# Optimization experiments

Measured on AMD Instinct MI355X. Metric: run time of the kernel, lower is better.

Reference implementation:

```python
import jax, jax.numpy as jnp
import numpy as np

N_CLASS = 12
N_OVO = N_CLASS * (N_CLASS - 1) // 2  # 66
_I_IDX, _J_IDX = np.triu_indices(N_CLASS, k=1)  # static pair -> (winner_if_pos, winner_if_neg)


def _resize_bilinear(x, size):
    # torch F.interpolate(mode='bilinear', align_corners=False) == jax half-pixel bilinear
    return jax.image.resize(x, (x.shape[0], x.shape[1], size, size), method='bilinear')


def _vote(o):
    # o: [N, n_ovo, H, W] pairwise logits -> [N, n_class, H, W] vote counts
    v = (o > 0).astype(o.dtype)                 # 1 where class i beats class j
    vt = jnp.swapaxes(v, 0, 1)                  # [P, N, H, W], pair axis leading
    res = (jax.ops.segment_sum(vt, jnp.asarray(_I_IDX), num_segments=N_CLASS)
           + jax.ops.segment_sum(1.0 - vt, jnp.asarray(_J_IDX), num_segments=N_CLASS))
    return jnp.swapaxes(res, 0, 1)              # [N, n_class, H, W]


def setup_inputs() -> dict:
    key = jax.random.key(0)
    ks = jax.random.split(key, 12)
    dims = [512, 256, 128, 64]
    sizes = [32, 64, 128, 256]
    N = 8
    inp = {}
    for i, (d, s) in enumerate(zip(dims, sizes)):
        inp[f"stage{i}"] = jax.random.normal(ks[i], (N, d, s, s), dtype=jnp.float32)
        inp[f"w{i}"] = jax.random.normal(ks[4 + i], (N_OVO, d), dtype=jnp.float32) * 0.05
        inp[f"b{i}"] = jax.random.normal(ks[8 + i], (N_OVO,), dtype=jnp.float32) * 0.05
    inp["last_only"] = 1
    return inp


def reference(stage0, stage1, stage2, stage3, w0, w1, w2, w3, b0, b1, b2, b3, last_only):
    stages = [stage0, stage1, stage2, stage3]
    ws = [w0, w1, w2, w3]
    bs = [b0, b1, b2, b3]
    # 1x1 convs: [N,C,H,W] x [O,C] -> [N,O,H,W]
    outputs = [jnp.einsum('nchw,oc->nohw', s, w) + b[None, :, None, None]
               for s, w, b in zip(stages, ws, bs)]
    if last_only:
        size = stages[-1].shape[2]
        total = outputs[0] * 0  # placeholder shape via sum below
        layers = [_resize_bilinear(o, size) for o in outputs]
        acc = layers[0]
        for l in layers[1:]:
            acc = acc + l
        outputs = [acc]
    else:
        for i in range(1, len(stages)):
            size = stages[i].shape[2]
            acc = outputs[i]
            for o in outputs[:i]:
                acc = acc + _resize_bilinear(o, size)
            outputs.append(acc)
    voted = tuple(_vote(o) for o in outputs)
    return voted[0] if last_only else voted
```

## Files before the change

### kernel.cpp

```cpp
#include <hip/hip_runtime.h>
#include <cstdint>
#include <cstddef>


#define N_BATCH 8
#define N_OVO   66
#define N_CLS   12

__constant__ unsigned char PAIR_I[N_OVO] = {
  0,0,0,0,0,0,0,0,0,0,0,
  1,1,1,1,1,1,1,1,1,1,
  2,2,2,2,2,2,2,2,2,
  3,3,3,3,3,3,3,3,
  4,4,4,4,4,4,4,
  5,5,5,5,5,5,
  6,6,6,6,6,
  7,7,7,7,
  8,8,8,
  9,9,
  10
};
__constant__ unsigned char PAIR_J[N_OVO] = {
  1,2,3,4,5,6,7,8,9,10,11,
  2,3,4,5,6,7,8,9,10,11,
  3,4,5,6,7,8,9,10,11,
  4,5,6,7,8,9,10,11,
  5,6,7,8,9,10,11,
  6,7,8,9,10,11,
  7,8,9,10,11,
  8,9,10,11,
  9,10,11,
  10,11,
  11
};

template<int C, int S2, int OG>
__device__ __forceinline__
void conv_body(int b, const float* __restrict__ x, const float* __restrict__ w,
               const float* __restrict__ bias, float* __restrict__ out)
{
    constexpr int NOG = N_OVO / OG;
    constexpr int PX  = S2 / 256;
    const int og  = b % NOG;
    int rest      = b / NOG;
    const int pxb = rest % PX;
    const int n   = rest / PX;
    const int o0  = og * OG;
    const int p   = pxb * 256 + threadIdx.x;

    float acc[OG];
#pragma unroll
    for (int oi = 0; oi < OG; ++oi) acc[oi] = 0.0f;

    const float* xb = x + (size_t)n * C * S2 + p;
    for (int c0 = 0; c0 < C; c0 += 8) {
        float xr[8];
#pragma unroll
        for (int k = 0; k < 8; ++k)
            xr[k] = xb[(size_t)(c0 + k) * S2];
#pragma unroll
        for (int oi = 0; oi < OG; ++oi) {
            const float* wrow = w + (size_t)(o0 + oi) * C + c0;
#pragma unroll
            for (int k = 0; k < 8; ++k)
                acc[oi] = __fmaf_rn(wrow[k], xr[k], acc[oi]);
        }
    }

    float* op = out + ((size_t)n * S2 + p) * N_OVO + o0;
#pragma unroll
    for (int oi = 0; oi < OG; ++oi)
        op[oi] = __fadd_rn(acc[oi], bias[o0 + oi]);
}

#define B0 192
#define B1 768
#define B2 3072

__global__ __launch_bounds__(256)
void conv_all(const float* __restrict__ x0, const float* __restrict__ w0,
              const float* __restrict__ b0, float* __restrict__ c0,
              const float* __restrict__ x1, const float* __restrict__ w1,
              const float* __restrict__ b1, float* __restrict__ c1,
              const float* __restrict__ x2, const float* __restrict__ w2,
              const float* __restrict__ b2, float* __restrict__ c2)
{
    const int bid = blockIdx.x;
    if (bid < B0) {
        conv_body<512, 1024, 11>(bid, x0, w0, b0, c0);
    } else if (bid < B0 + B1) {
        conv_body<256, 4096, 11>(bid - B0, x1, w1, b1, c1);
    } else {
        conv_body<128, 16384, 11>(bid - (B0 + B1), x2, w2, b2, c2);
    }
}

#define WT0 4
#define WT1 6
#define WT2 10

template<int WT, int SS>
__device__ __forceinline__ void stage_tile(float* __restrict__ t,
                                           const float* __restrict__ src,
                                           int y0, int x0)
{
    constexpr int RELS = WT * WT;
    for (int idx = threadIdx.x; idx < RELS * 33; idx += 256) {
        int r  = idx / 33;
        int k  = idx - r * 33;
        int ry = r / WT, rx = r - ry * WT;
        int sy = min(max(y0 + ry, 0), SS - 1);
        int sx = min(max(x0 + rx, 0), SS - 1);
        const float2 v = *reinterpret_cast<const float2*>(
            src + ((size_t)sy * SS + sx) * N_OVO + 2 * k);
        int dst = (k < 32) ? ((k >> 1) * (RELS * 4) + r * 4 + (k & 1) * 2)
                           : (64 * RELS + r * 2);
        *reinterpret_cast<float2*>(t + dst) = v;
    }
}

__device__ __forceinline__ float bil1(float v00, float v01, float v10, float v11,
                                      float wy, float wy0, float wx, float wx0,
                                      int ysing, int xsing)
{
    float u0 = ysing ? v00 : __fmaf_rn(wy, v10, __fmul_rn(wy0, v00));
    float u1 = ysing ? v01 : __fmaf_rn(wy, v11, __fmul_rn(wy0, v01));
    return xsing ? u0 : __fmaf_rn(wx, u1, __fmul_rn(wx0, u0));
}

template<int RELS>
__device__ __forceinline__ float4 bil4(const float* __restrict__ t, int g,
                                       int r00, int r01, int r10, int r11,
                                       float wy, float wx, int ysing, int xsing)
{
    const float* base = t + g * (RELS * 4);
    float4 v00 = *reinterpret_cast<const float4*>(base + r00 * 4);
    float4 v01 = *reinterpret_cast<const float4*>(base + r01 * 4);
    float4 v10 = *reinterpret_cast<const float4*>(base + r10 * 4);
    float4 v11 = *reinterpret_cast<const float4*>(base + r11 * 4);
    float wy0 = 1.0f - wy, wx0 = 1.0f - wx;
    float4 r;
    r.x = bil1(v00.x, v01.x, v10.x, v11.x, wy, wy0, wx, wx0, ysing, xsing);
    r.y = bil1(v00.y, v01.y, v10.y, v11.y, wy, wy0, wx, wx0, ysing, xsing);
    r.z = bil1(v00.z, v01.z, v10.z, v11.z, wy, wy0, wx, wx0, ysing, xsing);
    r.w = bil1(v00.w, v01.w, v10.w, v11.w, wy, wy0, wx, wx0, ysing, xsing);
    return r;
}

__global__ __launch_bounds__(256, 4)
void fuse_vote(const float* __restrict__ x3, const float* __restrict__ w3,
               const float* __restrict__ b3,
               const float* __restrict__ c0buf, const float* __restrict__ c1buf,
               const float* __restrict__ c2buf,
               float* __restrict__ out)
{
    const int n  = blockIdx.z;
    const int tx = threadIdx.x & 15, ty = threadIdx.x >> 4;
    const int X0 = blockIdx.x * 16,  Y0 = blockIdx.y * 16;
    const int X  = X0 + tx,          Y  = Y0 + ty;

    __shared__ alignas(16) float t0s[16  * N_OVO];
    __shared__ alignas(16) float t1s[36  * N_OVO];
    __shared__ alignas(16) float t2s[100 * N_OVO];

    int rel00[3], rel01[3], rel10[3], rel11[3], ysing[3], xsing[3];
    float wxv[3], wyv[3];
    int x0raw[3], y0raw[3];
    const int   Ss[3]   = {32, 64, 128};
    const float invs[3] = {32.0f / 256.0f, 64.0f / 256.0f, 128.0f / 256.0f};
    const int   Wt[3]   = {WT0, WT1, WT2};
#pragma unroll
    for (int s = 0; s < 3; ++s) {
        float inv = invs[s];
        int S = Ss[s];
        x0raw[s] = (int)floorf(((float)X0 + 0.5f) * inv - 0.5f);
        y0raw[s] = (int)floorf(((float)Y0 + 0.5f) * inv - 0.5f);
        float fx = ((float)X + 0.5f) * inv - 0.5f;
        float fy = ((float)Y + 0.5f) * inv - 0.5f;
        int ix0 = (int)floorf(fx), iy0 = (int)floorf(fy);
        wxv[s] = fx - (float)ix0;  wyv[s] = fy - (float)iy0;
        xsing[s] = (ix0 < 0) || (ix0 + 1 > S - 1);
        ysing[s] = (iy0 < 0) || (iy0 + 1 > S - 1);
        int rx = ix0 - x0raw[s], ry = iy0 - y0raw[s];
        rel00[s] = ry * Wt[s] + rx;
        rel01[s] = rel00[s] + 1;
        rel10[s] = rel00[s] + Wt[s];
        rel11[s] = rel10[s] + 1;
    }

    stage_tile<WT0, 32 >(t0s, c0buf + (size_t)n * 1024  * N_OVO, y0raw[0], x0raw[0]);
    stage_tile<WT1, 64 >(t1s, c1buf + (size_t)n * 4096  * N_OVO, y0raw[1], x0raw[1]);
    stage_tile<WT2, 128>(t2s, c2buf + (size_t)n * 16384 * N_OVO, y0raw[2], x0raw[2]);

    float xr[64];
    {
        const float* xp = x3 + (size_t)n * 64 * 65536 + (size_t)Y * 256 + X;
#pragma unroll
        for (int c = 0; c < 64; ++c) xr[c] = xp[(size_t)c * 65536];
    }

    __syncthreads();

    unsigned long long packed = 0;

#pragma unroll 1
    for (int g = 0; g < 16; ++g) {
        const int o = g * 4;
        float a0 = 0.0f, a1 = 0.0f, a2 = 0.0f, a3 = 0.0f;
        const float* wr0 = w3 + (size_t)o * 64;
        const float* wr1 = wr0 + 64;
        const float* wr2 = wr0 + 128;
        const float* wr3 = wr0 + 192;
#pragma unroll
        for (int c = 0; c < 64; ++c) {
            a0 = __fmaf_rn(wr0[c], xr[c], a0);
            a1 = __fmaf_rn(wr1[c], xr[c], a1);
            a2 = __fmaf_rn(wr2[c], xr[c], a2);
            a3 = __fmaf_rn(wr3[c], xr[c], a3);
        }
        float4 L3;
        L3.x = __fadd_rn(a0, b3[o]);
        L3.y = __fadd_rn(a1, b3[o + 1]);
        L3.z = __fadd_rn(a2, b3[o + 2]);
        L3.w = __fadd_rn(a3, b3[o + 3]);

        float4 s0 = bil4<16 >(t0s, g, rel00[0], rel01[0], rel10[0], rel11[0],
                              wyv[0], wxv[0], ysing[0], xsing[0]);
        float4 s1 = bil4<36 >(t1s, g, rel00[1], rel01[1], rel10[1], rel11[1],
                              wyv[1], wxv[1], ysing[1], xsing[1]);
        float4 s2 = bil4<100>(t2s, g, rel00[2], rel01[2], rel10[2], rel11[2],
                              wyv[2], wxv[2], ysing[2], xsing[2]);

        float v0 = __fadd_rn(__fadd_rn(__fadd_rn(s0.x, s1.x), s2.x), L3.x);
        float v1 = __fadd_rn(__fadd_rn(__fadd_rn(s0.y, s1.y), s2.y), L3.y);
        float v2 = __fadd_rn(__fadd_rn(__fadd_rn(s0.z, s1.z), s2.z), L3.z);
        float v3 = __fadd_rn(__fadd_rn(__fadd_rn(s0.w, s1.w), s2.w), L3.w);

        packed += (v0 > 0.0f) ? (1ull << (4 * (int)PAIR_I[o]))
                              : (1ull << (4 * (int)PAIR_J[o]));
        packed += (v1 > 0.0f) ? (1ull << (4 * (int)PAIR_I[o + 1]))
                              : (1ull << (4 * (int)PAIR_J[o + 1]));
        packed += (v2 > 0.0f) ? (1ull << (4 * (int)PAIR_I[o + 2]))
                              : (1ull << (4 * (int)PAIR_J[o + 2]));
        packed += (v3 > 0.0f) ? (1ull << (4 * (int)PAIR_I[o + 3]))
                              : (1ull << (4 * (int)PAIR_J[o + 3]));
    }

    {
        float a0 = 0.0f, a1 = 0.0f;
        const float* wr0 = w3 + (size_t)64 * 64;
        const float* wr1 = wr0 + 64;
#pragma unroll
        for (int c = 0; c < 64; ++c) {
            a0 = __fmaf_rn(wr0[c], xr[c], a0);
            a1 = __fmaf_rn(wr1[c], xr[c], a1);
        }
        float L3a = __fadd_rn(a0, b3[64]);
        float L3b = __fadd_rn(a1, b3[65]);

        float La[3], Lb[3];
#pragma unroll
        for (int s = 0; s < 3; ++s) {
            const float* t = (s == 0) ? t0s : (s == 1) ? t1s : t2s;
            const int RELS = Wt[s] * Wt[s];
            const float* tb = t + 64 * RELS;
            float2 v00 = *reinterpret_cast<const float2*>(tb + rel00[s] * 2);
            float2 v01 = *reinterpret_cast<const float2*>(tb + rel01[s] * 2);
            float2 v10 = *reinterpret_cast<const float2*>(tb + rel10[s] * 2);
            float2 v11 = *reinterpret_cast<const float2*>(tb + rel11[s] * 2);
            float wy = wyv[s], wx = wxv[s];
            float wy0 = 1.0f - wy, wx0 = 1.0f - wx;
            La[s] = bil1(v00.x, v01.x, v10.x, v11.x, wy, wy0, wx, wx0, ysing[s], xsing[s]);
            Lb[s] = bil1(v00.y, v01.y, v10.y, v11.y, wy, wy0, wx, wx0, ysing[s], xsing[s]);
        }
        float ta = __fadd_rn(__fadd_rn(__fadd_rn(La[0], La[1]), La[2]), L3a);
        float tb = __fadd_rn(__fadd_rn(__fadd_rn(Lb[0], Lb[1]), Lb[2]), L3b);
        packed += (ta > 0.0f) ? (1ull << (4 * (int)PAIR_I[64]))
                              : (1ull << (4 * (int)PAIR_J[64]));
        packed += (tb > 0.0f) ? (1ull << (4 * (int)PAIR_I[65]))
                              : (1ull << (4 * (int)PAIR_J[65]));
    }

    float* op = out + (size_t)n * N_CLS * 65536 + (size_t)Y * 256 + X;
#pragma unroll
    for (int k = 0; k < N_CLS; ++k)
        op[(size_t)k * 65536] = (float)(int)((packed >> (4 * k)) & 15ull);
}

extern "C" void kernel_launch(void* const* d_in, const int* in_sizes, int n_in,
                              void* d_out, int out_size, void* d_ws, size_t ws_size,
                              hipStream_t stream)
{
    const float* stage0 = (const float*)d_in[0];
    const float* w0     = (const float*)d_in[1];
    const float* b0     = (const float*)d_in[2];
    const float* stage1 = (const float*)d_in[3];
    const float* w1     = (const float*)d_in[4];
    const float* b1     = (const float*)d_in[5];
    const float* stage2 = (const float*)d_in[6];
    const float* w2     = (const float*)d_in[7];
    const float* b2     = (const float*)d_in[8];
    const float* stage3 = (const float*)d_in[9];
    const float* w3     = (const float*)d_in[10];
    const float* b3     = (const float*)d_in[11];
    float* out = (float*)d_out;

    float* c0 = (float*)d_ws;
    float* c1 = c0 + (size_t)540672;
    float* c2 = c1 + (size_t)2162688;

    conv_all<<<dim3(B0 + B1 + B2), 256, 0, stream>>>(
        stage0, w0, b0, c0,
        stage1, w1, b1, c1,
        stage2, w2, b2, c2);

    fuse_vote<<<dim3(16, 16, N_BATCH), 256, 0, stream>>>(stage3, w3, b3, c0, c1, c2, out);
}
```

Measured before the change: 487.0 us.

## Restructure stage3 conv as outer-product accumulation with transposed weights and swizzled LDS

The stage3 1x1 conv is reordered so that each thread streams its 64 input channels once and accumulates into 66 output registers. It reads the weights from a transposed global copy, which an extra block appended to the first kernel produces. The shared-memory tile layout gains an XOR swizzle on the relative pixel index, meant to reduce LDS bank conflicts on the bilinear float4 reads. The vote loop is now fully unrolled. The cost is a 66-float accumulator array per thread, which raises register pressure under the 4-waves occupancy bound and risks spills.

```diff
diff --git a/kernel.cpp b/kernel.cpp
--- a/kernel.cpp
+++ b/kernel.cpp
@@ -34,6 +34,8 @@
   11
 };
 
+__device__ float W3T[64 * N_OVO];
+
 template<int C, int S2, int OG>
 __device__ __forceinline__
 void conv_body(int b, const float* __restrict__ x, const float* __restrict__ w,
@@ -83,21 +85,28 @@
               const float* __restrict__ x1, const float* __restrict__ w1,
               const float* __restrict__ b1, float* __restrict__ c1,
               const float* __restrict__ x2, const float* __restrict__ w2,
-              const float* __restrict__ b2, float* __restrict__ c2)
+              const float* __restrict__ b2, float* __restrict__ c2,
+              const float* __restrict__ w3)
 {
     const int bid = blockIdx.x;
     if (bid < B0) {
         conv_body<512, 1024, 11>(bid, x0, w0, b0, c0);
     } else if (bid < B0 + B1) {
         conv_body<256, 4096, 11>(bid - B0, x1, w1, b1, c1);
+    } else if (bid < B0 + B1 + B2) {
+        conv_body<128, 16384, 11>(bid - (B0 + B1), x2, w2, b2, c2);
     } else {
-        conv_body<128, 16384, 11>(bid - (B0 + B1), x2, w2, b2, c2);
+        for (int idx = threadIdx.x; idx < 64 * N_OVO; idx += 256) {
+            int c = idx / N_OVO; int o = idx - c * N_OVO;
+            W3T[idx] = w3[o * 64 + c];
+        }
     }
 }
 
 #define WT0 4
 #define WT1 6
 #define WT2 10
+
 
 template<int WT, int SS>
 __device__ __forceinline__ void stage_tile(float* __restrict__ t,
@@ -113,8 +122,13 @@
         int sx = min(max(x0 + rx, 0), SS - 1);
         const float2 v = *reinterpret_cast<const float2*>(
             src + ((size_t)sy * SS + sx) * N_OVO + 2 * k);
-        int dst = (k < 32) ? ((k >> 1) * (RELS * 4) + r * 4 + (k & 1) * 2)
-                           : (64 * RELS + r * 2);
+        int dst;
+        if (k < 32) {
+            int sr = r ^ ((r >> 3) & 3);
+            dst = ((k >> 1) * RELS + sr) * 4 + (k & 1) * 2;
+        } else {
+            dst = 64 * RELS + r * 2;
+        }
         *reinterpret_cast<float2*>(t + dst) = v;
     }
 }
@@ -130,14 +144,14 @@
 
 template<int RELS>
 __device__ __forceinline__ float4 bil4(const float* __restrict__ t, int g,
-                                       int r00, int r01, int r10, int r11,
+                                       int s00, int s01, int s10, int s11,
                                        float wy, float wx, int ysing, int xsing)
 {
     const float* base = t + g * (RELS * 4);
-    float4 v00 = *reinterpret_cast<const float4*>(base + r00 * 4);
-    float4 v01 = *reinterpret_cast<const float4*>(base + r01 * 4);
-    float4 v10 = *reinterpret_cast<const float4*>(base + r10 * 4);
-    float4 v11 = *reinterpret_cast<const float4*>(base + r11 * 4);
+    float4 v00 = *reinterpret_cast<const float4*>(base + s00 * 4);
+    float4 v01 = *reinterpret_cast<const float4*>(base + s01 * 4);
+    float4 v10 = *reinterpret_cast<const float4*>(base + s10 * 4);
+    float4 v11 = *reinterpret_cast<const float4*>(base + s11 * 4);
     float wy0 = 1.0f - wy, wx0 = 1.0f - wx;
     float4 r;
     r.x = bil1(v00.x, v01.x, v10.x, v11.x, wy, wy0, wx, wx0, ysing, xsing);
@@ -148,7 +162,7 @@
 }
 
 __global__ __launch_bounds__(256, 4)
-void fuse_vote(const float* __restrict__ x3, const float* __restrict__ w3,
+void fuse_vote(const float* __restrict__ x3,
                const float* __restrict__ b3,
                const float* __restrict__ c0buf, const float* __restrict__ c1buf,
                const float* __restrict__ c2buf,
@@ -164,6 +178,7 @@
     __shared__ alignas(16) float t2s[100 * N_OVO];
 
     int rel00[3], rel01[3], rel10[3], rel11[3], ysing[3], xsing[3];
+    int s00[3], s01[3], s10[3], s11[3];
     float wxv[3], wyv[3];
     int x0raw[3], y0raw[3];
     const int   Ss[3]   = {32, 64, 128};
@@ -186,49 +201,50 @@
         rel01[s] = rel00[s] + 1;
         rel10[s] = rel00[s] + Wt[s];
         rel11[s] = rel10[s] + 1;
+        s00[s] = rel00[s] ^ ((rel00[s] >> 3) & 3);
+        s01[s] = rel01[s] ^ ((rel01[s] >> 3) & 3);
+        s10[s] = rel10[s] ^ ((rel10[s] >> 3) & 3);
+        s11[s] = rel11[s] ^ ((rel11[s] >> 3) & 3);
     }
 
     stage_tile<WT0, 32 >(t0s, c0buf + (size_t)n * 1024  * N_OVO, y0raw[0], x0raw[0]);
     stage_tile<WT1, 64 >(t1s, c1buf + (size_t)n * 4096  * N_OVO, y0raw[1], x0raw[1]);
     stage_tile<WT2, 128>(t2s, c2buf + (size_t)n * 16384 * N_OVO, y0raw[2], x0raw[2]);
 
-    float xr[64];
+    float acc[N_OVO];
+#pragma unroll
+    for (int o = 0; o < N_OVO; ++o) acc[o] = 0.0f;
+
     {
         const float* xp = x3 + (size_t)n * 64 * 65536 + (size_t)Y * 256 + X;
-#pragma unroll
-        for (int c = 0; c < 64; ++c) xr[c] = xp[(size_t)c * 65536];
+#pragma unroll 4
+        for (int c = 0; c < 64; ++c) {
+            float xv = xp[(size_t)c * 65536];
+            const float* wc = W3T + c * N_OVO;
+#pragma unroll
+            for (int o = 0; o < N_OVO; ++o)
+                acc[o] = __fmaf_rn(wc[o], xv, acc[o]);
+        }
     }
 
     __syncthreads();
 
     unsigned long long packed = 0;
 
-#pragma unroll 1
+#pragma unroll
     for (int g = 0; g < 16; ++g) {
         const int o = g * 4;
-        float a0 = 0.0f, a1 = 0.0f, a2 = 0.0f, a3 = 0.0f;
-        const float* wr0 = w3 + (size_t)o * 64;
-        const float* wr1 = wr0 + 64;
-        const float* wr2 = wr0 + 128;
-        const float* wr3 = wr0 + 192;
-#pragma unroll
-        for (int c = 0; c < 64; ++c) {
-            a0 = __fmaf_rn(wr0[c], xr[c], a0);
-            a1 = __fmaf_rn(wr1[c], xr[c], a1);
-            a2 = __fmaf_rn(wr2[c], xr[c], a2);
-            a3 = __fmaf_rn(wr3[c], xr[c], a3);
-        }
         float4 L3;
-        L3.x = __fadd_rn(a0, b3[o]);
-        L3.y = __fadd_rn(a1, b3[o + 1]);
-        L3.z = __fadd_rn(a2, b3[o + 2]);
-        L3.w = __fadd_rn(a3, b3[o + 3]);
-
-        float4 s0 = bil4<16 >(t0s, g, rel00[0], rel01[0], rel10[0], rel11[0],
+        L3.x = __fadd_rn(acc[o],     b3[o]);
+        L3.y = __fadd_rn(acc[o + 1], b3[o + 1]);
+        L3.z = __fadd_rn(acc[o + 2], b3[o + 2]);
+        L3.w = __fadd_rn(acc[o + 3], b3[o + 3]);
+
+        float4 s0 = bil4<16 >(t0s, g, s00[0], s01[0], s10[0], s11[0],
                               wyv[0], wxv[0], ysing[0], xsing[0]);
-        float4 s1 = bil4<36 >(t1s, g, rel00[1], rel01[1], rel10[1], rel11[1],
+        float4 s1 = bil4<36 >(t1s, g, s00[1], s01[1], s10[1], s11[1],
                               wyv[1], wxv[1], ysing[1], xsing[1]);
-        float4 s2 = bil4<100>(t2s, g, rel00[2], rel01[2], rel10[2], rel11[2],
+        float4 s2 = bil4<100>(t2s, g, s00[2], s01[2], s10[2], s11[2],
                               wyv[2], wxv[2], ysing[2], xsing[2]);
 
         float v0 = __fadd_rn(__fadd_rn(__fadd_rn(s0.x, s1.x), s2.x), L3.x);
@@ -247,16 +263,8 @@
     }
 
     {
-        float a0 = 0.0f, a1 = 0.0f;
-        const float* wr0 = w3 + (size_t)64 * 64;
-        const float* wr1 = wr0 + 64;
-#pragma unroll
-        for (int c = 0; c < 64; ++c) {
-            a0 = __fmaf_rn(wr0[c], xr[c], a0);
-            a1 = __fmaf_rn(wr1[c], xr[c], a1);
-        }
-        float L3a = __fadd_rn(a0, b3[64]);
-        float L3b = __fadd_rn(a1, b3[65]);
+        float L3a = __fadd_rn(acc[64], b3[64]);
+        float L3b = __fadd_rn(acc[65], b3[65]);
 
         float La[3], Lb[3];
 #pragma unroll
@@ -309,10 +317,11 @@
     float* c1 = c0 + (size_t)540672;
     float* c2 = c1 + (size_t)2162688;
 
-    conv_all<<<dim3(B0 + B1 + B2), 256, 0, stream>>>(
+    conv_all<<<dim3(B0 + B1 + B2 + 1), 256, 0, stream>>>(
         stage0, w0, b0, c0,
         stage1, w1, b1, c1,
-        stage2, w2, b2, c2);
-
-    fuse_vote<<<dim3(16, 16, N_BATCH), 256, 0, stream>>>(stage3, w3, b3, c0, c1, c2, out);
-}
+        stage2, w2, b2, c2,
+        w3);
+
+    fuse_vote<<<dim3(16, 16, N_BATCH), 256, 0, stream>>>(stage3, b3, c0, c1, c2, out);
+}
```

Result: no change. 484.6 us (-0.5%).
